# Kernel tuning notes

Hardware: AMD Instinct MI355X
Metric: run time of the kernel (lower is better)

The kernel has to match this reference:

```python
import jax, jax.numpy as jnp
import numpy as np
from jax import lax

B, C, H, W = 8, 256, 128, 128
RED = 4  # SE reduction


def setup_inputs() -> dict:
    key = jax.random.key(0)
    ks = jax.random.split(key, 7)
    s = 0.05
    return {
        "x": jax.random.normal(ks[0], (B, C, H, W), dtype=jnp.float32),
        "w_deform": jax.random.normal(ks[1], (C, C, 3, 3), dtype=jnp.float32) * s,
        "b_deform": jax.random.normal(ks[2], (C,), dtype=jnp.float32) * s,
        "w_se1": jax.random.normal(ks[3], (C // RED, C), dtype=jnp.float32) * s,
        "b_se1": jax.random.normal(ks[4], (C // RED,), dtype=jnp.float32) * s,
        "w_se2": jax.random.normal(ks[5], (C, C // RED), dtype=jnp.float32) * s,
        "b_se2": jax.random.normal(ks[6], (C,), dtype=jnp.float32) * s,
    }


def reference(x, w_deform, b_deform, w_se1, b_se1, w_se2, b_se2):
    # DeformConv2d with the all-zero offset tensor used in forward(): bilinear
    # sampling at integer taps == standard 3x3 conv, padding=1, zero-padded borders.
    y = lax.conv_general_dilated(
        x, w_deform,
        window_strides=(1, 1),
        padding=((1, 1), (1, 1)),
        dimension_numbers=("NCHW", "OIHW", "NCHW"),
    ) + b_deform[None, :, None, None]  # [B, C, H, W]

    # SE: global average pool -> 1x1 conv -> ReLU -> 1x1 conv -> sigmoid
    p = y.mean(axis=(2, 3))                                   # [B, C]
    h = jax.nn.relu(p @ w_se1.T + b_se1)                      # [B, C//RED]
    scale = jax.nn.sigmoid(h @ w_se2.T + b_se2)               # [B, C]
    return y * scale[:, :, None, None]
```

## Files before the change

kernel.cpp:

```cpp
#include <hip/hip_runtime.h>
#include <hip/hip_bf16.h>

#define BB 8
#define CC 256
#define HH 128
#define WW 128

typedef __attribute__((ext_vector_type(8))) short bf16x8;
typedef __attribute__((ext_vector_type(4))) float f32x4;

static __device__ __forceinline__ unsigned short f2bf(float f) {
  unsigned int u = __builtin_bit_cast(unsigned int, f);
  u += 0x7fffu + ((u >> 16) & 1u);
  return (unsigned short)(u >> 16);
}

static __device__ __forceinline__ void async16(const void* g, void* l) {
#if __has_builtin(__builtin_amdgcn_global_load_lds)
  __builtin_amdgcn_global_load_lds(
      (__attribute__((address_space(1))) void*)(unsigned long long)(g),
      (__attribute__((address_space(3))) void*)(unsigned int)(unsigned long long)(l),
      16, 0, 0);
#else
  *(bf16x8*)l = *(const bf16x8*)g;
#endif
}

__global__ __launch_bounds__(256) void k_convert_w(const float* __restrict__ w,
                                                   unsigned short* __restrict__ Wt) {
  __shared__ unsigned short lw[8 * 2304];
  const int t = threadIdx.x;
  const int co0 = blockIdx.x << 3;
  const float* src = w + co0 * 2304;
  for (int k = t; k < 18432; k += 256) lw[k] = f2bf(src[k]);
  __syncthreads();
  for (int g = t; g < 18432; g += 256) {
    const int tap = g >> 11, rem = g & 2047;
    const int o = rem >> 6, rem2 = rem & 63;
    const int cl = rem2 >> 3, e = rem2 & 7;
    Wt[(((tap << 5) + o) << 11) + ((co0 + cl) << 3) + e] =
        lw[cl * 2304 + ((o << 3) + e) * 9 + tap];
  }
}

__global__ __launch_bounds__(256) void k_transpose_x(const float* __restrict__ x,
                                                     unsigned short* __restrict__ Xc,
                                                     float* __restrict__ pS,
                                                     float* __restrict__ pC0,
                                                     float* __restrict__ pC1) {
  __shared__ float tile[64][130];
  const int t = threadIdx.x;
  const int bh = blockIdx.y;
  const int b = bh >> 7;
  const int c0 = blockIdx.x << 6;
  const float* xp = x + ((b * CC) * HH + (bh & 127)) * WW;
#pragma unroll
  for (int i = 0; i < 8; ++i) {
    int idx = t + (i << 8);
    int cr = idx >> 5, wq = idx & 31;
    float4 v = *(const float4*)(xp + (c0 + cr) * (HH * WW) + (wq << 2));
    tile[cr][(wq << 2) + 0] = v.x;
    tile[cr][(wq << 2) + 1] = v.y;
    tile[cr][(wq << 2) + 2] = v.z;
    tile[cr][(wq << 2) + 3] = v.w;
  }
  __syncthreads();
  const int ob = c0 >> 3;
#pragma unroll
  for (int i = 0; i < 4; ++i) {
    int g = t + (i << 8);
    int o = g >> 7, wr = g & 127;
    bf16x8 v;
#pragma unroll
    for (int e = 0; e < 8; ++e) v[e] = (short)f2bf(tile[(o << 3) + e][wr]);
    *(bf16x8*)(Xc + ((bh * 32) + ob + o) * 1024 + wr * 8) = v;
  }
  {
    const int c = t >> 2, seg = t & 3;
    float s = 0.f;
#pragma unroll
    for (int k = 0; k < 32; ++k)
      s += tile[c][(seg << 5) + ((k + (seg << 3)) & 31)];
    s += __shfl_xor(s, 1);
    s += __shfl_xor(s, 2);
    if (seg == 0) {
      const int idx = (bh << 8) + c0 + c;
      pS[idx]  = s;
      pC0[idx] = tile[c][0];
      pC1[idx] = tile[c][127];
    }
  }
}

__global__ __launch_bounds__(256) void k_pool2(const float* __restrict__ w,
                                               const float* __restrict__ bd,
                                               const float* __restrict__ pS,
                                               const float* __restrict__ pC0,
                                               const float* __restrict__ pC1,
                                               float* __restrict__ p_buf) {
  __shared__ float ts[2304];
  const int b = blockIdx.y, t = threadIdx.x;
  const int lane = t & 63, wid = t >> 6;
  {
    const int base = (b << 15) + t;
    float S = 0.f, C0 = 0.f, C1 = 0.f;
#pragma unroll 4
    for (int h = 0; h < 128; ++h) {
      S  += pS [base + (h << 8)];
      C0 += pC0[base + (h << 8)];
      C1 += pC1[base + (h << 8)];
    }
    const float R0 = pS[base],  R1 = pS[base + (127 << 8)];
    const float x00 = pC0[base], xH0 = pC0[base + (127 << 8)];
    const float x0W = pC1[base], xHW = pC1[base + (127 << 8)];
    const float er[3] = {R1, 0.f, R0};
    const float ec[3] = {C1, 0.f, C0};
    const float cor[9] = {xHW, 0.f, xH0, 0.f, 0.f, 0.f, x0W, 0.f, x00};
#pragma unroll
    for (int kh = 0; kh < 3; ++kh)
#pragma unroll
      for (int kw = 0; kw < 3; ++kw)
        ts[t * 9 + kh * 3 + kw] = S - er[kh] - ec[kw] + cor[kh * 3 + kw];
  }
  __syncthreads();
  float4 tv[9];
#pragma unroll
  for (int q = 0; q < 9; ++q) tv[q] = *(const float4*)&ts[(q * 64 + lane) * 4];
  const int co = (blockIdx.x << 3) + (wid << 1);
#pragma unroll
  for (int c2 = 0; c2 < 2; ++c2) {
    const float4* wr = (const float4*)(w + (co + c2) * 2304) + lane;
    float s = 0.f;
#pragma unroll
    for (int q = 0; q < 9; ++q) {
      float4 wv = wr[q * 64];
      s += wv.x * tv[q].x + wv.y * tv[q].y + wv.z * tv[q].z + wv.w * tv[q].w;
    }
    s += __shfl_xor(s, 1);  s += __shfl_xor(s, 2);  s += __shfl_xor(s, 4);
    s += __shfl_xor(s, 8);  s += __shfl_xor(s, 16); s += __shfl_xor(s, 32);
    if (lane == 0) p_buf[(b << 8) + co + c2] = bd[co + c2] + s * (1.0f / 16384.0f);
  }
}

__global__ __launch_bounds__(256) void k_se2(const float* __restrict__ p_buf,
                                             const float* __restrict__ w1,
                                             const float* __restrict__ b1,
                                             const float* __restrict__ w2,
                                             const float* __restrict__ b2,
                                             float* __restrict__ scale) {
  __shared__ float p[CC];
  __shared__ float h1[64];
  const int b = blockIdx.x, t = threadIdx.x;
  const int lane = t & 63, wid = t >> 6;
  p[t] = p_buf[(b << 8) + t];
  __syncthreads();
  {
    const float4 pv = *(const float4*)&p[lane << 2];
#pragma unroll
    for (int i = 0; i < 16; ++i) {
      const int r = (wid << 4) + i;
      float4 wv = ((const float4*)(w1 + (r << 8)))[lane];
      float s = wv.x * pv.x + wv.y * pv.y + wv.z * pv.z + wv.w * pv.w;
      s += __shfl_xor(s, 1);  s += __shfl_xor(s, 2);  s += __shfl_xor(s, 4);
      s += __shfl_xor(s, 8);  s += __shfl_xor(s, 16); s += __shfl_xor(s, 32);
      if (lane == 0) {
        float v = b1[r] + s;
        h1[r] = v > 0.f ? v : 0.f;
      }
    }
  }
  __syncthreads();
  {
    float s = b2[t];
    const float* wr = w2 + (t << 6);
#pragma unroll
    for (int k = 0; k < 64; ++k) s += wr[k] * h1[k];
    scale[(b << 8) + t] = 1.0f / (1.0f + expf(-s));
  }
}

__global__ __launch_bounds__(256, 2) void k_conv(
    const unsigned short* __restrict__ Xc, const unsigned short* __restrict__ Wt,
    const float* __restrict__ bias, const float* __restrict__ scale,
    float* __restrict__ out) {
  extern __shared__ __align__(16) unsigned short Xs[];
  const int t = threadIdx.x;
  const int lin = (blockIdx.y << 1) | blockIdx.x;
  const int Wk = ((lin & 7) << 7) | (lin >> 3);
  const int m0 = (Wk & 1) << 7;
  const int bhp = Wk >> 1;
  const int b = bhp >> 6;
  const int h0 = (bhp & 63) << 1;
  const int lane = t & 63, wid = t >> 6;
  const int wave_m = (wid & 1) << 6, wave_n = (wid >> 1) << 6;
  const int n0 = lane & 15, quad = lane >> 4;
  const int part = wid & 1, rsel = wid >> 1;

  bf16x8 z8 = {0, 0, 0, 0, 0, 0, 0, 0};
  if (t < 64) {
    int bi = t >> 5, rem = t & 31;
    int dh = rem >> 3, rem2 = rem & 7, q = rem2 >> 1, side = rem2 & 1;
    *(bf16x8*)&Xs[bi * 16640 + dh * 4160 + q * 1040 + (side ? 1032 : 0)] = z8;
  }
  if (h0 == 0 || h0 == 126) {
    const int dhz = (h0 == 0) ? 0 : 3;
    for (int g = t; g < 1040; g += 256) {
      int bi = g >= 520, gg = g - bi * 520;
      *(bf16x8*)&Xs[bi * 16640 + dhz * 4160 + gg * 8] = z8;
    }
  }

  auto stage = [&](int cb8, int bi) {
    const int ob = cb8 << 2;
#pragma unroll
    for (int r = 0; r < 8; ++r) {
      const int rr = (r << 1) | rsel;
      const int dh = rr >> 2, q = rr & 3;
      const int hh = h0 - 1 + dh;
      if (hh >= 0 && hh < HH) {
        const unsigned short* gp =
            Xc + ((((b << 7) + hh) * 32 + ob + q) << 10) + (part << 9) + (lane << 3);
        unsigned short* lp =
            &Xs[bi * 16640 + dh * 4160 + q * 1040 + 8 + (part << 9) + (lane << 3)];
        async16(gp, lp);
      }
    }
  };

  f32x4 acc[2][4][4];
  f32x4 zero4 = {0.f, 0.f, 0.f, 0.f};
#pragma unroll
  for (int r = 0; r < 2; ++r)
#pragma unroll
    for (int i = 0; i < 4; ++i)
#pragma unroll
      for (int j = 0; j < 4; ++j) acc[r][i][j] = zero4;

  stage(0, 0);
  __syncthreads();

  for (int cb8 = 0; cb8 < 8; ++cb8) {
    const int cur = cb8 & 1;
    if (cb8 < 7) stage(cb8 + 1, cur ^ 1);
    const unsigned short* wb =
        Wt + ((((cb8 << 2) + quad) << 8) + m0 + wave_m + n0) * 8;
    const unsigned short* xb = &Xs[cur * 16640 + quad * 1040 + (wave_n + n0) * 8];

    bf16x8 af[3][4], bg[2][4];
#pragma unroll
    for (int i = 0; i < 4; ++i) af[0][i] = *(const bf16x8*)(wb + 0 * 65536 + i * 128);
#pragma unroll
    for (int i = 0; i < 4; ++i) af[1][i] = *(const bf16x8*)(wb + 3 * 65536 + i * 128);
#pragma unroll
    for (int j = 0; j < 4; ++j) bg[0][j] = *(const bf16x8*)(xb + (j << 4) * 8);

#pragma unroll
    for (int kw = 0; kw < 3; ++kw) {
#pragma unroll
      for (int dh = 0; dh < 4; ++dh) {
        const int s = (kw << 2) + dh;
        if (s < 11) {
          const int sn = s + 1, kwn = sn >> 2, dhn = sn & 3;
#pragma unroll
          for (int j = 0; j < 4; ++j)
            bg[sn & 1][j] =
                *(const bf16x8*)(xb + dhn * 4160 + (((j << 4) + kwn)) * 8);
        }
        __builtin_amdgcn_s_setprio(1);
        if (dh >= 1) {
          const int p1 = kw * 3 + dh - 1;
#pragma unroll
          for (int i = 0; i < 4; ++i)
#pragma unroll
            for (int j = 0; j < 4; ++j)
              acc[1][i][j] = __builtin_amdgcn_mfma_f32_16x16x32_bf16(
                  af[p1 % 3][i], bg[s & 1][j], acc[1][i][j], 0, 0, 0);
        }
        if (dh <= 2) {
          const int p0 = kw * 3 + dh;
#pragma unroll
          for (int i = 0; i < 4; ++i)
#pragma unroll
            for (int j = 0; j < 4; ++j)
              acc[0][i][j] = __builtin_amdgcn_mfma_f32_16x16x32_bf16(
                  af[p0 % 3][i], bg[s & 1][j], acc[0][i][j], 0, 0, 0);
        }
        __builtin_amdgcn_s_setprio(0);
        if (s >= 1 && s <= 7) {
          const int pn = s + 1;
          const int tapn = (pn % 3) * 3 + pn / 3;
#pragma unroll
          for (int i = 0; i < 4; ++i)
            af[pn % 3][i] = *(const bf16x8*)(wb + tapn * 65536 + i * 128);
        }
      }
    }
    __syncthreads();
  }

#pragma unroll
  for (int i = 0; i < 4; ++i) {
    const int mrow = m0 + wave_m + (i << 4) + (quad << 2);
    float bs[4], ss[4];
#pragma unroll
    for (int r4 = 0; r4 < 4; ++r4) {
      bs[r4] = bias[mrow + r4];
      ss[r4] = scale[(b << 8) + mrow + r4];
    }
#pragma unroll
    for (int r = 0; r < 2; ++r)
#pragma unroll
      for (int j = 0; j < 4; ++j) {
        const int wcol = wave_n + (j << 4) + n0;
        float* op = out + ((((b << 8) + mrow) * HH) + h0 + r) * WW + wcol;
#pragma unroll
        for (int r4 = 0; r4 < 4; ++r4)
          op[r4 * (HH * WW)] = (acc[r][i][j][r4] + bs[r4]) * ss[r4];
      }
  }
}

extern "C" void kernel_launch(void* const* d_in, const int* in_sizes, int n_in,
                              void* d_out, int out_size, void* d_ws, size_t ws_size,
                              hipStream_t stream) {
  const float* x  = (const float*)d_in[0];
  const float* wd = (const float*)d_in[1];
  const float* bd = (const float*)d_in[2];
  const float* w1 = (const float*)d_in[3];
  const float* b1 = (const float*)d_in[4];
  const float* w2 = (const float*)d_in[5];
  const float* b2 = (const float*)d_in[6];
  float* out = (float*)d_out;

  char* ws = (char*)d_ws;
  unsigned short* Xc = (unsigned short*)ws;
  unsigned short* Wt = (unsigned short*)(ws + 67108864);
  float* p_buf = (float*)(ws + 68362240);
  float* scale = (float*)(ws + 68370432);

  float* pS  = out;
  float* pC0 = out + 262144;
  float* pC1 = out + 524288;

  (void)hipFuncSetAttribute((const void*)k_conv,
                            hipFuncAttributeMaxDynamicSharedMemorySize, 66560);

  k_convert_w<<<dim3(32), dim3(256), 0, stream>>>(wd, Wt);
  k_transpose_x<<<dim3(4, 1024), dim3(256), 0, stream>>>(x, Xc, pS, pC0, pC1);
  k_pool2<<<dim3(32, 8), dim3(256), 0, stream>>>(wd, bd, pS, pC0, pC1, p_buf);
  k_se2<<<dim3(8), dim3(256), 0, stream>>>(p_buf, w1, b1, w2, b2, scale);
  k_conv<<<dim3(2, 512), dim3(256), 66560, stream>>>(Xc, Wt, bd, scale, out);
}
```

Measured before the change: 381.4 us.

## Merge preprocessing kernels, fold SE MLP into conv, delay next-stage prefetch

Merges the weight-conversion and x-transpose kernels into one launch, with a block-index branch choosing the role. Drops the separate SE kernel: each conv block now recomputes the SE MLP for its batch from the pooled vector and keeps the scale in shared memory. The async staging of the next channel block is moved from the top of the loop into the middle of the tap loop. This removes two launches and a global scale round trip, at the cost of redundant MLP work in every conv block, slightly more LDS, and a different load/compute overlap.

```diff
diff --git a/kernel.cpp b/kernel.cpp
--- a/kernel.cpp
+++ b/kernel.cpp
@@ -26,33 +26,37 @@
 #endif
 }
 
-__global__ __launch_bounds__(256) void k_convert_w(const float* __restrict__ w,
-                                                   unsigned short* __restrict__ Wt) {
-  __shared__ unsigned short lw[8 * 2304];
+__global__ __launch_bounds__(256) void k_pre(const float* __restrict__ x,
+                                             const float* __restrict__ w,
+                                             unsigned short* __restrict__ Xc,
+                                             unsigned short* __restrict__ Wt,
+                                             float* __restrict__ pS,
+                                             float* __restrict__ pC0,
+                                             float* __restrict__ pC1) {
+  __shared__ __align__(16) unsigned char smem[36864];
   const int t = threadIdx.x;
-  const int co0 = blockIdx.x << 3;
-  const float* src = w + co0 * 2304;
-  for (int k = t; k < 18432; k += 256) lw[k] = f2bf(src[k]);
-  __syncthreads();
-  for (int g = t; g < 18432; g += 256) {
-    const int tap = g >> 11, rem = g & 2047;
-    const int o = rem >> 6, rem2 = rem & 63;
-    const int cl = rem2 >> 3, e = rem2 & 7;
-    Wt[(((tap << 5) + o) << 11) + ((co0 + cl) << 3) + e] =
-        lw[cl * 2304 + ((o << 3) + e) * 9 + tap];
-  }
-}
-
-__global__ __launch_bounds__(256) void k_transpose_x(const float* __restrict__ x,
-                                                     unsigned short* __restrict__ Xc,
-                                                     float* __restrict__ pS,
-                                                     float* __restrict__ pC0,
-                                                     float* __restrict__ pC1) {
-  __shared__ float tile[64][130];
-  const int t = threadIdx.x;
-  const int bh = blockIdx.y;
+  const int bx = blockIdx.x;
+
+  if (bx >= 4096) {
+    unsigned short* lw = (unsigned short*)smem;
+    const int co0 = (bx - 4096) << 3;
+    const float* src = w + co0 * 2304;
+    for (int k = t; k < 18432; k += 256) lw[k] = f2bf(src[k]);
+    __syncthreads();
+    for (int g = t; g < 18432; g += 256) {
+      const int tap = g >> 11, rem = g & 2047;
+      const int o = rem >> 6, rem2 = rem & 63;
+      const int cl = rem2 >> 3, e = rem2 & 7;
+      Wt[(((tap << 5) + o) << 11) + ((co0 + cl) << 3) + e] =
+          lw[cl * 2304 + ((o << 3) + e) * 9 + tap];
+    }
+    return;
+  }
+
+  float (*tile)[130] = (float(*)[130])smem;
+  const int bh = bx >> 2;
   const int b = bh >> 7;
-  const int c0 = blockIdx.x << 6;
+  const int c0 = (bx & 3) << 6;
   const float* xp = x + ((b * CC) * HH + (bh & 127)) * WW;
 #pragma unroll
   for (int i = 0; i < 8; ++i) {
@@ -142,48 +146,16 @@
   }
 }
 
-__global__ __launch_bounds__(256) void k_se2(const float* __restrict__ p_buf,
-                                             const float* __restrict__ w1,
-                                             const float* __restrict__ b1,
-                                             const float* __restrict__ w2,
-                                             const float* __restrict__ b2,
-                                             float* __restrict__ scale) {
-  __shared__ float p[CC];
-  __shared__ float h1[64];
-  const int b = blockIdx.x, t = threadIdx.x;
-  const int lane = t & 63, wid = t >> 6;
-  p[t] = p_buf[(b << 8) + t];
-  __syncthreads();
-  {
-    const float4 pv = *(const float4*)&p[lane << 2];
-#pragma unroll
-    for (int i = 0; i < 16; ++i) {
-      const int r = (wid << 4) + i;
-      float4 wv = ((const float4*)(w1 + (r << 8)))[lane];
-      float s = wv.x * pv.x + wv.y * pv.y + wv.z * pv.z + wv.w * pv.w;
-      s += __shfl_xor(s, 1);  s += __shfl_xor(s, 2);  s += __shfl_xor(s, 4);
-      s += __shfl_xor(s, 8);  s += __shfl_xor(s, 16); s += __shfl_xor(s, 32);
-      if (lane == 0) {
-        float v = b1[r] + s;
-        h1[r] = v > 0.f ? v : 0.f;
-      }
-    }
-  }
-  __syncthreads();
-  {
-    float s = b2[t];
-    const float* wr = w2 + (t << 6);
-#pragma unroll
-    for (int k = 0; k < 64; ++k) s += wr[k] * h1[k];
-    scale[(b << 8) + t] = 1.0f / (1.0f + expf(-s));
-  }
-}
-
 __global__ __launch_bounds__(256, 2) void k_conv(
     const unsigned short* __restrict__ Xc, const unsigned short* __restrict__ Wt,
-    const float* __restrict__ bias, const float* __restrict__ scale,
+    const float* __restrict__ bias, const float* __restrict__ p_buf,
+    const float* __restrict__ w1, const float* __restrict__ b1,
+    const float* __restrict__ w2, const float* __restrict__ b2,
     float* __restrict__ out) {
   extern __shared__ __align__(16) unsigned short Xs[];
+  float* p_lds = (float*)(Xs + 33280);
+  float* h1s   = p_lds + 256;
+  float* sc    = h1s + 64;
   const int t = threadIdx.x;
   const int lin = (blockIdx.y << 1) | blockIdx.x;
   const int Wk = ((lin & 7) << 7) | (lin >> 3);
@@ -237,11 +209,36 @@
       for (int j = 0; j < 4; ++j) acc[r][i][j] = zero4;
 
   stage(0, 0);
+
+  p_lds[t] = p_buf[(b << 8) + t];
+  __syncthreads();
+  {
+    const float4 pv = *(const float4*)&p_lds[lane << 2];
+#pragma unroll
+    for (int i = 0; i < 16; ++i) {
+      const int r = (wid << 4) + i;
+      float4 wv = ((const float4*)(w1 + (r << 8)))[lane];
+      float s = wv.x * pv.x + wv.y * pv.y + wv.z * pv.z + wv.w * pv.w;
+      s += __shfl_xor(s, 1);  s += __shfl_xor(s, 2);  s += __shfl_xor(s, 4);
+      s += __shfl_xor(s, 8);  s += __shfl_xor(s, 16); s += __shfl_xor(s, 32);
+      if (lane == 0) {
+        float v = b1[r] + s;
+        h1s[r] = v > 0.f ? v : 0.f;
+      }
+    }
+  }
+  __syncthreads();
+  if (t < 128) {
+    float s2 = b2[m0 + t];
+    const float* wr2 = w2 + ((m0 + t) << 6);
+#pragma unroll
+    for (int k = 0; k < 64; ++k) s2 += wr2[k] * h1s[k];
+    sc[t] = 1.0f / (1.0f + expf(-s2));
+  }
   __syncthreads();
 
   for (int cb8 = 0; cb8 < 8; ++cb8) {
     const int cur = cb8 & 1;
-    if (cb8 < 7) stage(cb8 + 1, cur ^ 1);
     const unsigned short* wb =
         Wt + ((((cb8 << 2) + quad) << 8) + m0 + wave_m + n0) * 8;
     const unsigned short* xb = &Xs[cur * 16640 + quad * 1040 + (wave_n + n0) * 8];
@@ -266,6 +263,7 @@
             bg[sn & 1][j] =
                 *(const bf16x8*)(xb + dhn * 4160 + (((j << 4) + kwn)) * 8);
         }
+        if (s == 8 && cb8 < 7) stage(cb8 + 1, cur ^ 1);
         __builtin_amdgcn_s_setprio(1);
         if (dh >= 1) {
           const int p1 = kw * 3 + dh - 1;
@@ -300,12 +298,13 @@
 
 #pragma unroll
   for (int i = 0; i < 4; ++i) {
-    const int mrow = m0 + wave_m + (i << 4) + (quad << 2);
+    const int mloc = wave_m + (i << 4) + (quad << 2);
+    const int mrow = m0 + mloc;
     float bs[4], ss[4];
 #pragma unroll
     for (int r4 = 0; r4 < 4; ++r4) {
       bs[r4] = bias[mrow + r4];
-      ss[r4] = scale[(b << 8) + mrow + r4];
+      ss[r4] = sc[mloc + r4];
     }
 #pragma unroll
     for (int r = 0; r < 2; ++r)
@@ -336,18 +335,16 @@
   unsigned short* Xc = (unsigned short*)ws;
   unsigned short* Wt = (unsigned short*)(ws + 67108864);
   float* p_buf = (float*)(ws + 68362240);
-  float* scale = (float*)(ws + 68370432);
 
   float* pS  = out;
   float* pC0 = out + 262144;
   float* pC1 = out + 524288;
 
   (void)hipFuncSetAttribute((const void*)k_conv,
-                            hipFuncAttributeMaxDynamicSharedMemorySize, 66560);
-
-  k_convert_w<<<dim3(32), dim3(256), 0, stream>>>(wd, Wt);
-  k_transpose_x<<<dim3(4, 1024), dim3(256), 0, stream>>>(x, Xc, pS, pC0, pC1);
+                            hipFuncAttributeMaxDynamicSharedMemorySize, 68352);
+
+  k_pre<<<dim3(4128), dim3(256), 0, stream>>>(x, wd, Xc, Wt, pS, pC0, pC1);
   k_pool2<<<dim3(32, 8), dim3(256), 0, stream>>>(wd, bd, pS, pC0, pC1, p_buf);
-  k_se2<<<dim3(8), dim3(256), 0, stream>>>(p_buf, w1, b1, w2, b2, scale);
-  k_conv<<<dim3(2, 512), dim3(256), 66560, stream>>>(Xc, Wt, bd, scale, out);
-}
+  k_conv<<<dim3(2, 512), dim3(256), 68352, stream>>>(Xc, Wt, bd, p_buf,
+                                                     w1, b1, w2, b2, out);
+}
```

Result: slower. 456.2 us (+19.6%).
